# Optimization experiments

Measured on AMD Instinct MI355X. Metric: run time of the kernel, lower is better.

The kernel has to match this reference:

```python
import jax, jax.numpy as jnp
import numpy as np

DIM = 1024
HEADS = 16
DIM_HEAD = 64
INNER = HEADS * DIM_HEAD  # 1024
SCALE = DIM_HEAD ** -0.5


def setup_inputs() -> dict:
    key = jax.random.key(0)
    k0, k1, k2 = jax.random.split(key, 3)
    x = jax.random.normal(k0, (4, 2048, DIM), dtype=jnp.float32)
    ln_gamma = jnp.ones((DIM,), dtype=jnp.float32)
    ln_beta = jnp.zeros((DIM,), dtype=jnp.float32)
    w_qkv = jax.random.normal(k1, (DIM, 3 * INNER), dtype=jnp.float32) * (DIM ** -0.5)
    w_out = jax.random.normal(k2, (INNER, DIM), dtype=jnp.float32) * (INNER ** -0.5)
    b_out = jnp.zeros((DIM,), dtype=jnp.float32)
    return {"x": x, "ln_gamma": ln_gamma, "ln_beta": ln_beta,
            "w_qkv": w_qkv, "w_out": w_out, "b_out": b_out}


def reference(x, ln_gamma, ln_beta, w_qkv, w_out, b_out):
    # LayerNorm over last dim (eps matches torch default 1e-5)
    mu = jnp.mean(x, axis=-1, keepdims=True)
    var = jnp.mean(jnp.square(x - mu), axis=-1, keepdims=True)
    xn = (x - mu) * jax.lax.rsqrt(var + 1e-5) * ln_gamma + ln_beta
    # QKV projection (no bias)
    qkv = xn @ w_qkv  # [b, t, 3*inner]
    q, k, v = jnp.split(qkv, 3, axis=-1)
    B, T, _ = x.shape
    def to_heads(t):
        return t.reshape(B, T, HEADS, DIM_HEAD).transpose(0, 2, 1, 3)  # b h t d
    q, k, v = to_heads(q), to_heads(k), to_heads(v)
    dots = jnp.einsum('bhid,bhjd->bhij', q, k) * SCALE
    attn = jax.nn.softmax(dots, axis=-1)
    out = jnp.einsum('bhij,bhjd->bhid', attn, v)
    out = out.transpose(0, 2, 1, 3).reshape(B, T, INNER)
    return out @ w_out + b_out
```

## Files before the change

kernel.cpp:

```cpp
#include <hip/hip_runtime.h>


#define DIMX 1024
#define TSEQ 2048
#define NB 4
#define NH 16
#define DH 64
#define NROWS (NB * TSEQ)
#define QSCALE 0.18033688011112042f

typedef __bf16 bf16_t;
typedef __bf16 bf16x8 __attribute__((ext_vector_type(8)));
typedef __bf16 bf16x4 __attribute__((ext_vector_type(4)));
typedef float f32x4 __attribute__((ext_vector_type(4)));

#if __has_builtin(__builtin_amdgcn_exp2f)
#define EXP2F __builtin_amdgcn_exp2f
#else
#define EXP2F exp2f
#endif

__device__ __forceinline__ bf16x4 cvt4(f32x4 v) {
    return __builtin_convertvector(v, bf16x4);
}
__device__ __forceinline__ void async16(const bf16_t* g, bf16_t* l) {
    __builtin_amdgcn_global_load_lds(
        (const __attribute__((address_space(1))) unsigned int*)g,
        (__attribute__((address_space(3))) unsigned int*)l, 16, 0, 0);
}

__global__ __launch_bounds__(256) void ln_kernel(
    const float* __restrict__ x, const float* __restrict__ g,
    const float* __restrict__ b, bf16_t* __restrict__ xn) {
    int row = blockIdx.x, tid = threadIdx.x;
    const float4 xv = *(const float4*)(x + (size_t)row * DIMX + tid * 4);
    float s = xv.x + xv.y + xv.z + xv.w;
    float q = xv.x * xv.x + xv.y * xv.y + xv.z * xv.z + xv.w * xv.w;
    for (int o = 32; o > 0; o >>= 1) {
        s += __shfl_xor(s, o);
        q += __shfl_xor(q, o);
    }
    __shared__ float2 red[4];
    int wave = tid >> 6, lane = tid & 63;
    if (lane == 0) red[wave] = make_float2(s, q);
    __syncthreads();
    float2 r0 = red[0], r1 = red[1], r2 = red[2], r3 = red[3];
    s = r0.x + r1.x + r2.x + r3.x;
    q = r0.y + r1.y + r2.y + r3.y;
    float mu = s * (1.0f / DIMX);
    float var = q * (1.0f / DIMX) - mu * mu;
    float rstd = rsqrtf(var + 1e-5f);
    float4 gv = *(const float4*)(g + tid * 4);
    float4 bv = *(const float4*)(b + tid * 4);
    f32x4 r;
    r[0] = (xv.x - mu) * rstd * gv.x + bv.x;
    r[1] = (xv.y - mu) * rstd * gv.y + bv.y;
    r[2] = (xv.z - mu) * rstd * gv.z + bv.z;
    r[3] = (xv.w - mu) * rstd * gv.w + bv.w;
    *(bf16x4*)(xn + (size_t)row * DIMX + tid * 4) = cvt4(r);
}

__global__ __launch_bounds__(256) void transpose_cast(
    const float* __restrict__ src, bf16_t* __restrict__ dst, int R, int C) {
    __shared__ float tile[32][33];
    int c0 = blockIdx.x * 32, r0 = blockIdx.y * 32;
    int tx = threadIdx.x, ty = threadIdx.y;
    for (int i = ty; i < 32; i += 8)
        tile[i][tx] = src[(size_t)(r0 + i) * C + c0 + tx];
    __syncthreads();
    for (int i = ty; i < 32; i += 8)
        dst[(size_t)(c0 + i) * R + r0 + tx] = (bf16_t)tile[tx][i];
}

#define MFMA16 __builtin_amdgcn_mfma_f32_16x16x32_bf16

template <int MODE>
__global__ __launch_bounds__(512, 2) void gemm256(
    const bf16_t* __restrict__ A, const bf16_t* __restrict__ BT,
    void* __restrict__ Cout, const float* __restrict__ bias, int M, int N, int K) {
    __shared__ __align__(16) bf16_t As[2][256 * 64];
    __shared__ __align__(16) bf16_t Bs[2][256 * 64];
    int tid = threadIdx.x, lane = tid & 63, wave = tid >> 6;
    int lm = lane & 15, quad = lane >> 4;
    int wr = wave >> 2, wc = wave & 3;

    int nbx = gridDim.x;
    int nwg = nbx * gridDim.y;
    int linear = blockIdx.y * nbx + blockIdx.x;
    int cpx = nwg >> 3;
    int swz = (linear & 7) * cpx + (linear >> 3);
    int bx = swz % nbx, by = swz / nbx;
    int m0 = by * 256, n0 = bx * 256;

    int srow = tid >> 3, sc8 = tid & 7;
    int scol = (sc8 ^ (srow & 7)) << 3;
    const bf16_t* ga = A + (size_t)(m0 + srow) * K + scol;
    const bf16_t* gb = BT + (size_t)(n0 + srow) * K + scol;
    int ldst = tid << 3;

    int sw0 = ((quad ^ (lm & 7)) << 3);
    int sw1 = (((4 + quad) ^ (lm & 7)) << 3);

    f32x4 zero = {0.f, 0.f, 0.f, 0.f};
    f32x4 acc[8][4];
#pragma unroll
    for (int i = 0; i < 8; ++i)
#pragma unroll
        for (int j = 0; j < 4; ++j) acc[i][j] = zero;

#pragma unroll
    for (int i = 0; i < 4; ++i) async16(ga + (size_t)i * 64 * K, &As[0][i * 4096 + ldst]);
#pragma unroll
    for (int i = 0; i < 4; ++i) async16(gb + (size_t)i * 64 * K, &Bs[0][i * 4096 + ldst]);
    asm volatile("s_waitcnt vmcnt(0)" ::: "memory");
    __builtin_amdgcn_s_barrier();

    int nkt = K >> 6;
    for (int kt = 0; kt < nkt; ++kt) {
        int c = kt & 1;
        int k1 = (kt + 1) << 6;
        bool pf = (kt + 1) < nkt;
        const bf16_t* pa = &As[c][0];
        const bf16_t* pb = &Bs[c][0];
        bf16_t* na = &As[c ^ 1][0];
        bf16_t* nb = &Bs[c ^ 1][0];
        bf16x8 af[4][2], bfr[2][2];

#pragma unroll
        for (int t = 0; t < 4; ++t) {
            int ro = (wr * 128 + t * 16 + lm) * 64;
            af[t][0] = *(const bf16x8*)&pa[ro + sw0];
            af[t][1] = *(const bf16x8*)&pa[ro + sw1];
        }
#pragma unroll
        for (int t = 0; t < 2; ++t) {
            int ro = (wc * 64 + t * 16 + lm) * 64;
            bfr[t][0] = *(const bf16x8*)&pb[ro + sw0];
            bfr[t][1] = *(const bf16x8*)&pb[ro + sw1];
        }
        if (pf) {
#pragma unroll
            for (int i = 0; i < 4; ++i)
                async16(ga + (size_t)i * 64 * K + k1, &na[i * 4096 + ldst]);
        }
        __builtin_amdgcn_s_barrier();
        asm volatile("s_waitcnt lgkmcnt(0)" ::: "memory");
        __builtin_amdgcn_s_setprio(1);
#pragma unroll
        for (int mt = 0; mt < 4; ++mt)
#pragma unroll
            for (int nt = 0; nt < 2; ++nt) {
                acc[mt][nt] = MFMA16(af[mt][0], bfr[nt][0], acc[mt][nt], 0, 0, 0);
                acc[mt][nt] = MFMA16(af[mt][1], bfr[nt][1], acc[mt][nt], 0, 0, 0);
            }
        __builtin_amdgcn_s_setprio(0);
        __builtin_amdgcn_s_barrier();

#pragma unroll
        for (int t = 0; t < 2; ++t) {
            int ro = (wc * 64 + (2 + t) * 16 + lm) * 64;
            bfr[t][0] = *(const bf16x8*)&pb[ro + sw0];
            bfr[t][1] = *(const bf16x8*)&pb[ro + sw1];
        }
        if (pf) {
#pragma unroll
            for (int i = 0; i < 4; ++i)
                async16(gb + (size_t)i * 64 * K + k1, &nb[i * 4096 + ldst]);
        }
        __builtin_amdgcn_s_barrier();
        asm volatile("s_waitcnt lgkmcnt(0)" ::: "memory");
        __builtin_amdgcn_s_setprio(1);
#pragma unroll
        for (int mt = 0; mt < 4; ++mt)
#pragma unroll
            for (int nt = 0; nt < 2; ++nt) {
                acc[mt][2 + nt] = MFMA16(af[mt][0], bfr[nt][0], acc[mt][2 + nt], 0, 0, 0);
                acc[mt][2 + nt] = MFMA16(af[mt][1], bfr[nt][1], acc[mt][2 + nt], 0, 0, 0);
            }
        __builtin_amdgcn_s_setprio(0);
        __builtin_amdgcn_s_barrier();

#pragma unroll
        for (int t = 0; t < 4; ++t) {
            int ro = (wr * 128 + (4 + t) * 16 + lm) * 64;
            af[t][0] = *(const bf16x8*)&pa[ro + sw0];
            af[t][1] = *(const bf16x8*)&pa[ro + sw1];
        }
        __builtin_amdgcn_s_barrier();
        asm volatile("s_waitcnt lgkmcnt(0)" ::: "memory");
        __builtin_amdgcn_s_setprio(1);
#pragma unroll
        for (int mt = 0; mt < 4; ++mt)
#pragma unroll
            for (int nt = 0; nt < 2; ++nt) {
                acc[4 + mt][2 + nt] = MFMA16(af[mt][0], bfr[nt][0], acc[4 + mt][2 + nt], 0, 0, 0);
                acc[4 + mt][2 + nt] = MFMA16(af[mt][1], bfr[nt][1], acc[4 + mt][2 + nt], 0, 0, 0);
            }
        __builtin_amdgcn_s_setprio(0);
        __builtin_amdgcn_s_barrier();

#pragma unroll
        for (int t = 0; t < 2; ++t) {
            int ro = (wc * 64 + t * 16 + lm) * 64;
            bfr[t][0] = *(const bf16x8*)&pb[ro + sw0];
            bfr[t][1] = *(const bf16x8*)&pb[ro + sw1];
        }
        __builtin_amdgcn_s_barrier();
        asm volatile("s_waitcnt lgkmcnt(0)" ::: "memory");
        __builtin_amdgcn_s_setprio(1);
#pragma unroll
        for (int mt = 0; mt < 4; ++mt)
#pragma unroll
            for (int nt = 0; nt < 2; ++nt) {
                acc[4 + mt][nt] = MFMA16(af[mt][0], bfr[nt][0], acc[4 + mt][nt], 0, 0, 0);
                acc[4 + mt][nt] = MFMA16(af[mt][1], bfr[nt][1], acc[4 + mt][nt], 0, 0, 0);
            }
        __builtin_amdgcn_s_setprio(0);
        asm volatile("s_waitcnt vmcnt(0)" ::: "memory");
        __builtin_amdgcn_s_barrier();
    }

#pragma unroll
    for (int mt = 0; mt < 8; ++mt) {
#pragma unroll
        for (int nt = 0; nt < 4; ++nt) {
            int m = m0 + wr * 128 + mt * 16 + quad * 4;
            int n = n0 + wc * 64 + nt * 16 + lm;
            if (MODE == 1) {
                int sel = n >> 10, nn = n & 1023, h = nn >> 6, d = nn & 63;
                int b = m >> 11, t = m & 2047;
                if (sel == 2) {
                    *(bf16x4*)((bf16_t*)Cout + (size_t)2 * 8388608 +
                               ((size_t)((b * NH + h) * DH + d)) * TSEQ + t) = cvt4(acc[mt][nt]);
                } else {
                    f32x4 sv = acc[mt][nt] * (sel == 0 ? QSCALE : 1.0f);
                    bf16x4 c4 = cvt4(sv);
#pragma unroll
                    for (int r = 0; r < 4; ++r)
                        ((bf16_t*)Cout)[(size_t)sel * 8388608 +
                                        ((size_t)((b * NH + h) * TSEQ + t + r)) * DH + d] = c4[r];
                }
            } else {
                float bn = bias[n];
#pragma unroll
                for (int r = 0; r < 4; ++r)
                    ((float*)Cout)[(size_t)(m + r) * N + n] = acc[mt][nt][r] + bn;
            }
        }
    }
}

__global__ __launch_bounds__(512, 4) void attn_mfma(
    const bf16_t* __restrict__ qkv, bf16_t* __restrict__ o) {
    int bh = blockIdx.y;
    int qt = blockIdx.x;
    const bf16_t* qb = qkv + (size_t)bh * TSEQ * DH;
    const bf16_t* kb = qkv + (size_t)8388608 + (size_t)bh * TSEQ * DH;
    const bf16_t* vb = qkv + (size_t)16777216 + (size_t)bh * DH * TSEQ;
    int tid = threadIdx.x, wave = tid >> 6, lane = tid & 63;
    int lm = lane & 15, quad = lane >> 4, lx = lm & 7;

    __shared__ __align__(16) bf16_t Ks[2][64 * 64];
    __shared__ __align__(16) bf16_t Vt[2][64 * 64];
    __shared__ __align__(16) bf16_t Ps[8 * 1024];

    int roff = tid >> 3;
    int cperm = ((tid & 7) ^ (roff & 7)) * 8;
    const bf16_t* kp = kb + (size_t)roff * DH + cperm;
    const bf16_t* vp = vb + (size_t)roff * TSEQ + cperm;
    int l0 = tid * 8;

    bf16x8 qf[2][2];
#pragma unroll
    for (int u = 0; u < 2; ++u)
#pragma unroll
        for (int ks = 0; ks < 2; ++ks)
            qf[u][ks] = *(const bf16x8*)(qb +
                (size_t)(qt * 256 + wave * 32 + u * 16 + lm) * DH + ks * 32 + quad * 8);

    f32x4 zero = {0.f, 0.f, 0.f, 0.f};
    f32x4 m16 = {-16.f, -16.f, -16.f, -16.f};
    f32x4 acc[2][4];
#pragma unroll
    for (int u = 0; u < 2; ++u)
#pragma unroll
        for (int dt = 0; dt < 4; ++dt) acc[u][dt] = zero;
    f32x4 l4[2] = {zero, zero};

    int fo0 = (quad ^ lx) * 8;
    int fo1 = ((4 + quad) ^ lx) * 8;
    int pb = wave * 1024 + lm * 64;

    async16(kp, &Ks[0][l0]);
    async16(vp, &Vt[0][l0]);
    kp += 64 * DH; vp += 64;
    asm volatile("s_waitcnt vmcnt(0)" ::: "memory");
    __builtin_amdgcn_s_barrier();

    for (int jt = 0; jt < TSEQ / 64; ++jt) {
        int c = jt & 1;
        if (jt + 1 < TSEQ / 64) {
            async16(kp, &Ks[c ^ 1][l0]);
            async16(vp, &Vt[c ^ 1][l0]);
            kp += 64 * DH; vp += 64;
        }

        bf16x8 kf[4][2];
#pragma unroll
        for (int nt = 0; nt < 4; ++nt) {
            kf[nt][0] = *(const bf16x8*)&Ks[c][(nt * 16 + lm) * 64 + fo0];
            kf[nt][1] = *(const bf16x8*)&Ks[c][(nt * 16 + lm) * 64 + fo1];
        }

        bf16x8 pf[2][2];
#pragma unroll
        for (int u = 0; u < 2; ++u) {
            f32x4 s[4];
            __builtin_amdgcn_s_setprio(1);
#pragma unroll
            for (int nt = 0; nt < 4; ++nt) {
                s[nt] = __builtin_amdgcn_mfma_f32_16x16x32_bf16(kf[nt][0], qf[u][0], m16, 0, 0, 0);
                s[nt] = __builtin_amdgcn_mfma_f32_16x16x32_bf16(kf[nt][1], qf[u][1], s[nt], 0, 0, 0);
            }
            __builtin_amdgcn_s_setprio(0);
#pragma unroll
            for (int nt = 0; nt < 4; ++nt) {
                f32x4 p;
#pragma unroll
                for (int e = 0; e < 4; ++e) p[e] = EXP2F(s[nt][e]);
                l4[u] += p;
                *(bf16x4*)&Ps[pb + ((nt * 2 + (quad >> 1)) ^ lx) * 8 + (quad & 1) * 4] = cvt4(p);
            }
            pf[u][0] = *(const bf16x8*)&Ps[pb + fo0];
            pf[u][1] = *(const bf16x8*)&Ps[pb + fo1];
        }

        __builtin_amdgcn_s_setprio(1);
#pragma unroll
        for (int dt = 0; dt < 4; ++dt) {
            bf16x8 vf0 = *(const bf16x8*)&Vt[c][(dt * 16 + lm) * 64 + fo0];
            bf16x8 vf1 = *(const bf16x8*)&Vt[c][(dt * 16 + lm) * 64 + fo1];
#pragma unroll
            for (int u = 0; u < 2; ++u) {
                acc[u][dt] = __builtin_amdgcn_mfma_f32_16x16x32_bf16(vf0, pf[u][0], acc[u][dt], 0, 0, 0);
                acc[u][dt] = __builtin_amdgcn_mfma_f32_16x16x32_bf16(vf1, pf[u][1], acc[u][dt], 0, 0, 0);
            }
        }
        __builtin_amdgcn_s_setprio(0);

        asm volatile("s_waitcnt vmcnt(0)" ::: "memory");
        __builtin_amdgcn_s_barrier();
    }

    int b = bh >> 4, h = bh & 15;
#pragma unroll
    for (int u = 0; u < 2; ++u) {
        float l = (l4[u][0] + l4[u][1]) + (l4[u][2] + l4[u][3]);
        l += __shfl_xor(l, 16);
        l += __shfl_xor(l, 32);
        float rl = 1.0f / l;
        int t = qt * 256 + wave * 32 + u * 16 + lm;
#pragma unroll
        for (int dt = 0; dt < 4; ++dt) {
            f32x4 ov = acc[u][dt] * rl;
            *(bf16x4*)(o + ((size_t)(b * TSEQ + t)) * DIMX + h * DH + dt * 16 + quad * 4) = cvt4(ov);
        }
    }
}

extern "C" void kernel_launch(void* const* d_in, const int* in_sizes, int n_in,
                              void* d_out, int out_size, void* d_ws, size_t ws_size,
                              hipStream_t stream) {
    const float* x = (const float*)d_in[0];
    const float* g = (const float*)d_in[1];
    const float* be = (const float*)d_in[2];
    const float* w_qkv = (const float*)d_in[3];
    const float* w_out = (const float*)d_in[4];
    const float* b_out = (const float*)d_in[5];
    float* out = (float*)d_out;
    char* ws = (char*)d_ws;

    bf16_t* xn = (bf16_t*)(ws);
    bf16_t* wqkvT = (bf16_t*)(ws + 16777216);
    bf16_t* woutT = (bf16_t*)(ws + 23068672);
    bf16_t* qkv = (bf16_t*)(ws + 25165824);
    bf16_t* attno = (bf16_t*)(ws + 75497472);

    ln_kernel<<<NROWS, 256, 0, stream>>>(x, g, be, xn);
    transpose_cast<<<dim3(96, 32), dim3(32, 8), 0, stream>>>(w_qkv, wqkvT, 1024, 3072);
    transpose_cast<<<dim3(32, 32), dim3(32, 8), 0, stream>>>(w_out, woutT, 1024, 1024);
    gemm256<1><<<dim3(12, 32), 512, 0, stream>>>(xn, wqkvT, (void*)qkv, nullptr, NROWS, 3072, 1024);
    attn_mfma<<<dim3(8, 64), 512, 0, stream>>>(qkv, attno);
    gemm256<2><<<dim3(4, 32), 512, 0, stream>>>(attno, woutT, (void*)out, b_out, NROWS, 1024, 1024);
}
```

Baseline: 290.0 us.

## Keep softmax probabilities in registers by permuting K rows and V columns

Removes the per-wave LDS buffer used to transpose the exp'd scores into the B-operand layout of the PV MFMA. The K rows each lane loads are remapped so the score accumulator's element order already matches the P fragment, and the V columns are remapped to match. P can then be built by packing registers. This drops LDS writes, reads and the shared-memory footprint, at the cost of a changed swizzle for the K/V async loads that must stay correct and conflict-free.

Result: no change. 285.2 us (-1.7%).

```diff
diff --git a/kernel.cpp b/kernel.cpp
--- a/kernel.cpp
+++ b/kernel.cpp
@@ -262,10 +262,10 @@
 
     __shared__ __align__(16) bf16_t Ks[2][64 * 64];
     __shared__ __align__(16) bf16_t Vt[2][64 * 64];
-    __shared__ __align__(16) bf16_t Ps[8 * 1024];
 
     int roff = tid >> 3;
-    int cperm = ((tid & 7) ^ (roff & 7)) * 8;
+    int fr = (roff & 3) | ((roff & 8) >> 1);
+    int cperm = ((tid & 7) ^ fr) * 8;
     const bf16_t* kp = kb + (size_t)roff * DH + cperm;
     const bf16_t* vp = vb + (size_t)roff * TSEQ + cperm;
     int l0 = tid * 8;
@@ -287,9 +287,16 @@
         for (int dt = 0; dt < 4; ++dt) acc[u][dt] = zero;
     f32x4 l4[2] = {zero, zero};
 
+    int qh = lm >> 2, rr = lm & 3;
+    int krow0 = 8 * qh + rr;
+    int krow1 = krow0 + 4;
+    int krow2 = 32 + 8 * (qh ^ 2) + rr;
+    int krow3 = krow2 + 4;
     int fo0 = (quad ^ lx) * 8;
     int fo1 = ((4 + quad) ^ lx) * 8;
-    int pb = wave * 1024 + lm * 64;
+    int fv = (lm & 3) | ((lm & 8) >> 1);
+    int vo0 = (quad ^ fv) * 8;
+    int vo1 = ((4 | (quad ^ 2)) ^ fv) * 8;
 
     async16(kp, &Ks[0][l0]);
     async16(vp, &Vt[0][l0]);
@@ -306,11 +313,14 @@
         }
 
         bf16x8 kf[4][2];
-#pragma unroll
-        for (int nt = 0; nt < 4; ++nt) {
-            kf[nt][0] = *(const bf16x8*)&Ks[c][(nt * 16 + lm) * 64 + fo0];
-            kf[nt][1] = *(const bf16x8*)&Ks[c][(nt * 16 + lm) * 64 + fo1];
-        }
+        kf[0][0] = *(const bf16x8*)&Ks[c][krow0 * 64 + fo0];
+        kf[0][1] = *(const bf16x8*)&Ks[c][krow0 * 64 + fo1];
+        kf[1][0] = *(const bf16x8*)&Ks[c][krow1 * 64 + fo0];
+        kf[1][1] = *(const bf16x8*)&Ks[c][krow1 * 64 + fo1];
+        kf[2][0] = *(const bf16x8*)&Ks[c][krow2 * 64 + fo0];
+        kf[2][1] = *(const bf16x8*)&Ks[c][krow2 * 64 + fo1];
+        kf[3][0] = *(const bf16x8*)&Ks[c][krow3 * 64 + fo0];
+        kf[3][1] = *(const bf16x8*)&Ks[c][krow3 * 64 + fo1];
 
         bf16x8 pf[2][2];
 #pragma unroll
@@ -323,23 +333,23 @@
                 s[nt] = __builtin_amdgcn_mfma_f32_16x16x32_bf16(kf[nt][1], qf[u][1], s[nt], 0, 0, 0);
             }
             __builtin_amdgcn_s_setprio(0);
+            f32x4 p[4];
 #pragma unroll
             for (int nt = 0; nt < 4; ++nt) {
-                f32x4 p;
-#pragma unroll
-                for (int e = 0; e < 4; ++e) p[e] = EXP2F(s[nt][e]);
-                l4[u] += p;
-                *(bf16x4*)&Ps[pb + ((nt * 2 + (quad >> 1)) ^ lx) * 8 + (quad & 1) * 4] = cvt4(p);
-            }
-            pf[u][0] = *(const bf16x8*)&Ps[pb + fo0];
-            pf[u][1] = *(const bf16x8*)&Ps[pb + fo1];
+#pragma unroll
+                for (int e = 0; e < 4; ++e) p[nt][e] = EXP2F(s[nt][e]);
+                l4[u] += p[nt];
+            }
+            bf16x4 c0 = cvt4(p[0]), c1 = cvt4(p[1]), c2 = cvt4(p[2]), c3 = cvt4(p[3]);
+            pf[u][0] = __builtin_shufflevector(c0, c1, 0, 1, 2, 3, 4, 5, 6, 7);
+            pf[u][1] = __builtin_shufflevector(c2, c3, 0, 1, 2, 3, 4, 5, 6, 7);
         }
 
         __builtin_amdgcn_s_setprio(1);
 #pragma unroll
         for (int dt = 0; dt < 4; ++dt) {
-            bf16x8 vf0 = *(const bf16x8*)&Vt[c][(dt * 16 + lm) * 64 + fo0];
-            bf16x8 vf1 = *(const bf16x8*)&Vt[c][(dt * 16 + lm) * 64 + fo1];
+            bf16x8 vf0 = *(const bf16x8*)&Vt[c][(dt * 16 + lm) * 64 + vo0];
+            bf16x8 vf1 = *(const bf16x8*)&Vt[c][(dt * 16 + lm) * 64 + vo1];
 #pragma unroll
             for (int u = 0; u < 2; ++u) {
                 acc[u][dt] = __builtin_amdgcn_mfma_f32_16x16x32_bf16(vf0, pf[u][0], acc[u][dt], 0, 0, 0);
```
